# Performance work log

Measured on AMD Instinct MI355X. Metric: run time of the kernel, lower is better.

Reference implementation:

```python
import jax, jax.numpy as jnp
import numpy as np

EPS = 1e-6


def _normalize(A):
    # zero the diagonal, then symmetric degree normalization D @ A @ D.
    # D is diagonal with 1/(eps + sqrt(rowsum)), so D@A@D is an
    # elementwise row/column scale (same math, no NxN diag matmuls).
    N = A.shape[-1]
    A = A * (1.0 - jnp.eye(N, dtype=A.dtype))          # [B,N,N]
    d = 1.0 / (EPS + jnp.sqrt(jnp.sum(A, axis=2)))     # [B,N]
    return d[:, :, None] * A * d[:, None, :]           # [B,N,N]


def setup_inputs() -> dict:
    key = jax.random.key(0)
    k1, k2, k3, k4 = jax.random.split(key, 4)
    B, N, F, K, out_dim = 16, 2048, 64, 4, 128
    X = jax.random.uniform(k1, (B, N, F), dtype=jnp.float32)
    A = jax.random.uniform(k2, (B, N, N), dtype=jnp.float32)
    kernel = jax.random.normal(k3, (K * F, out_dim), dtype=jnp.float32) * 0.05
    bias = jax.random.normal(k4, (out_dim,), dtype=jnp.float32) * 0.05
    return {"X": X, "A": A, "kernel": kernel, "bias": bias}


def reference(X, A, kernel, bias):
    K = 4
    L = _normalize(A)                                  # [B,N,N]
    Xt = [X, jnp.matmul(L, X)]                         # T0, T1
    for k in range(2, K):
        Xt.append(2.0 * jnp.matmul(L, Xt[k - 1]) - Xt[k - 2])
    out = jnp.concatenate(Xt, axis=-1)                 # [B,N,K*F]
    out = jnp.matmul(out, kernel) + bias               # [B,N,out_dim]
    return jax.nn.relu(out)
```

## Files before the change

### kernel.cpp

```cpp
#include <hip/hip_runtime.h>

typedef __attribute__((ext_vector_type(4))) float  f32x4;
typedef __attribute__((ext_vector_type(8))) short  bf16x8;
typedef __attribute__((ext_vector_type(4))) int    i32x4;
typedef __attribute__((ext_vector_type(4))) unsigned short u16x4;
typedef __attribute__((ext_vector_type(8))) unsigned short u16x8;

#define NB 16
#define NN 2048
#define FF 64

#define INV_SCALE (1.0f / (127.0f * 131072.0f))

__device__ __forceinline__ unsigned short f2bf(float x) {
  union { float f; unsigned int u; } c; c.f = x;
  unsigned int u = c.u;
  return (unsigned short)((u + 0x7fffu + ((u >> 16) & 1u)) >> 16);
}
__device__ __forceinline__ float bf2f(unsigned short b) {
  union { unsigned int u; float f; } c; c.u = (unsigned int)b << 16;
  return c.f;
}

__device__ __forceinline__ void gload16(const void* g, void* l) {
  __builtin_amdgcn_global_load_lds(
      (const __attribute__((address_space(1))) void*)g,
      (__attribute__((address_space(3))) void*)l, 16, 0, 0);
}

#define BAR() asm volatile("s_barrier" ::: "memory")

__global__ __launch_bounds__(256) void rowsum_conv_kernel(
    const float* __restrict__ A, char* __restrict__ A8,
    float* __restrict__ dvec) {
  int row = blockIdx.x * 4 + (threadIdx.x >> 6);
  int lane = threadIdx.x & 63;
  int i = row & (NN - 1);
  const float* arow = A + (size_t)row * NN;
  char* orow = A8 + (size_t)row * NN;
  float s = 0.f;
#pragma unroll
  for (int p = 0; p < 8; ++p) {
    int base = p * 256 + lane * 4;
    f32x4 v = __builtin_nontemporal_load((const f32x4*)(arow + base));
#pragma unroll
    for (int jj = 0; jj < 4; ++jj) if (base + jj == i) v[jj] = 0.f;
    s += v[0] + v[1] + v[2] + v[3];
    unsigned int q0 = (unsigned int)(int)rintf(v[0] * 127.f);
    unsigned int q1 = (unsigned int)(int)rintf(v[1] * 127.f);
    unsigned int q2 = (unsigned int)(int)rintf(v[2] * 127.f);
    unsigned int q3 = (unsigned int)(int)rintf(v[3] * 127.f);
    unsigned int w8 = (q0 & 255u) | ((q1 & 255u) << 8) |
                      ((q2 & 255u) << 16) | ((q3 & 255u) << 24);
    *(unsigned int*)(orow + base) = w8;
  }
#pragma unroll
  for (int off = 32; off > 0; off >>= 1) s += __shfl_down(s, off, 64);
  if (lane == 0) dvec[row] = 1.0f / (1e-6f + sqrtf(s));
}

__global__ __launch_bounds__(256) void scale_transpose_kernel(
    const float* __restrict__ V, const float* __restrict__ dvec,
    char* __restrict__ Uh, char* __restrict__ Ul,
    unsigned short* __restrict__ Tb,
    const float* __restrict__ Kr, unsigned short* __restrict__ WT) {
  int bid = blockIdx.x;
  int tid = threadIdx.x;
  if (bid >= 512) {
    int idx = (bid - 512) * 256 + tid;
    int k = idx >> 7, c = idx & 127;
    WT[c * 256 + k] = f2bf(Kr[idx]);
    return;
  }
  int b = bid >> 5;
  int n0 = (bid & 31) * 64;
  __shared__ float t[64][65];
#pragma unroll
  for (int it = 0; it < 4; ++it) {
    int e = it * 256 + tid;
    int nl = e >> 4;
    int f0 = (e & 15) * 4;
    int n = n0 + nl;
    f32x4 v = *(const f32x4*)&V[((size_t)b * NN + n) * FF + f0];
    float dd = dvec[b * NN + n];
    u16x4 o;
#pragma unroll
    for (int j = 0; j < 4; ++j) { o[j] = f2bf(v[j]); t[f0 + j][nl] = v[j] * dd; }
    *(u16x4*)&Tb[((size_t)b * NN + n) * FF + f0] = o;
  }
  __syncthreads();
#pragma unroll
  for (int it = 0; it < 2; ++it) {
    int c = it * 256 + tid;
    int f = c >> 3, nl0 = (c & 7) * 8;
    unsigned long long ph = 0, pl = 0;
#pragma unroll
    for (int j = 0; j < 8; ++j) {
      int q = (int)rintf(t[f][nl0 + j] * 131072.f);
      q = q > 16383 ? 16383 : (q < -16383 ? -16383 : q);
      ph |= (unsigned long long)((unsigned int)(q >> 7) & 255u) << (8 * j);
      pl |= (unsigned long long)((unsigned int)(q & 127)) << (8 * j);
    }
    size_t o = ((size_t)b * FF + f) * NN + n0 + nl0;
    *(unsigned long long*)&Uh[o] = ph;
    *(unsigned long long*)&Ul[o] = pl;
  }
}

__global__ __launch_bounds__(256) void cheb_mm_kernel(
    const char* __restrict__ A8,
    const char* __restrict__ Uh,
    const char* __restrict__ Ul,
    const float* __restrict__ dvec,
    const unsigned short* __restrict__ prevb,
    unsigned short* __restrict__ Tbout,
    char* __restrict__ Uhout,
    char* __restrict__ Ulout,
    float cs) {
  __shared__ char lds[36864];
  int bid = blockIdx.x;
  int slot = bid >> 3;
  int b = (bid & 7) * 2 + (slot >> 5);
  int tm = slot & 31;
  int tid = threadIdx.x;
  int lane = tid & 63;
  int w = tid >> 6;
  int wm = w >> 1, wn = w & 1;
  int lr = lane >> 2;
  int gs = (lane & 3) ^ (lr & 3);
  int r16 = lane & 15, kq = lane >> 4;
  const int NT = NN / 64;

  const size_t abase = ((size_t)b * NN + (size_t)tm * 64) * NN;
  const size_t ubase = (size_t)b * FF * NN;

  i32x4 ach[2][2] = {};
  i32x4 acl[2][2] = {};

  auto stage = [&](int s, int kt) {
    int k0 = kt * 64;
    int r = w * 16 + lr;
    gload16(A8 + abase + (size_t)r * NN + k0 + gs * 16,
            &lds[s * 4096 + w * 1024]);
    gload16(Uh + ubase + (size_t)r * NN + k0 + gs * 16,
            &lds[12288 + s * 4096 + w * 1024]);
    gload16(Ul + ubase + (size_t)r * NN + k0 + gs * 16,
            &lds[24576 + s * 4096 + w * 1024]);
  };

  stage(0, 0); stage(1, 1); stage(2, 2);
  int s = 0;
  for (int t = 0; t < NT; ++t) {
    if (t < NT - 2)       asm volatile("s_waitcnt vmcnt(6)" ::: "memory");
    else if (t == NT - 2) asm volatile("s_waitcnt vmcnt(3)" ::: "memory");
    else                  asm volatile("s_waitcnt vmcnt(0)" ::: "memory");
    BAR();
    i32x4 af[2], uhf[2], ulf[2];
#pragma unroll
    for (int mi = 0; mi < 2; ++mi) {
      int row = wm * 32 + mi * 16 + r16;
      af[mi] = *(const i32x4*)&lds[s * 4096 + row * 64 + ((kq ^ (row & 3)) * 16)];
    }
#pragma unroll
    for (int ni = 0; ni < 2; ++ni) {
      int fr = wn * 32 + ni * 16 + r16;
      uhf[ni] = *(const i32x4*)&lds[12288 + s * 4096 + fr * 64 + ((kq ^ (fr & 3)) * 16)];
      ulf[ni] = *(const i32x4*)&lds[24576 + s * 4096 + fr * 64 + ((kq ^ (fr & 3)) * 16)];
    }
#pragma unroll
    for (int mi = 0; mi < 2; ++mi)
#pragma unroll
      for (int ni = 0; ni < 2; ++ni) {
        ach[mi][ni] = __builtin_amdgcn_mfma_i32_16x16x64_i8(
            af[mi], uhf[ni], ach[mi][ni], 0, 0, 0);
        acl[mi][ni] = __builtin_amdgcn_mfma_i32_16x16x64_i8(
            af[mi], ulf[ni], acl[mi][ni], 0, 0, 0);
      }
    BAR();
    if (t + 3 < NT) stage(s, t + 3);
    s = (s == 2) ? 0 : s + 1;
  }

  char (*th)[72]  = (char(*)[72])lds;
  char (*tlo)[72] = (char(*)[72])&lds[12288];
  int n0 = tm * 64;
#pragma unroll
  for (int mi = 0; mi < 2; ++mi) {
#pragma unroll
    for (int r = 0; r < 4; ++r) {
      int rl = wm * 32 + mi * 16 + kq * 4 + r;
      int row = n0 + rl;
      float dd = dvec[b * NN + row];
      float dcs = dd * cs;
#pragma unroll
      for (int ni = 0; ni < 2; ++ni) {
        int col = wn * 32 + ni * 16 + r16;
        size_t idx = ((size_t)b * NN + row) * FF + col;
        float c = 128.f * (float)ach[mi][ni][r] + (float)acl[mi][ni][r];
        float v = dcs * c;
        if (prevb) v -= bf2f(prevb[idx]);
        Tbout[idx] = f2bf(v);
        if (Uhout) {
          int q = (int)rintf(dd * v * 131072.f);
          q = q > 16383 ? 16383 : (q < -16383 ? -16383 : q);
          th[col][rl]  = (char)(q >> 7);
          tlo[col][rl] = (char)(q & 127);
        }
      }
    }
  }
  if (Uhout) {
    __syncthreads();
#pragma unroll
    for (int it = 0; it < 2; ++it) {
      int c = tid + it * 256;
      int f = c >> 3, nl0 = (c & 7) * 8;
      unsigned long long vh = *(const unsigned long long*)&th[f][nl0];
      unsigned long long vl = *(const unsigned long long*)&tlo[f][nl0];
      size_t o = ((size_t)b * FF + f) * NN + n0 + nl0;
      *(unsigned long long*)&Uhout[o] = vh;
      *(unsigned long long*)&Ulout[o] = vl;
    }
  }
}

__global__ __launch_bounds__(256) void final_gemm_kernel(
    const unsigned short* __restrict__ Tb,
    const unsigned short* __restrict__ WT,
    const float* __restrict__ bias,
    float* __restrict__ out) {
  __shared__ unsigned short lds[36864];
  const int M = NB * NN;
  int m0 = blockIdx.x * 64;
  int tid = threadIdx.x;
  int lane = tid & 63, w = tid >> 6;
  int wm = w >> 1, wn = w & 1;
  int lr = lane >> 3, gs = (lane & 7) ^ lr;
  int r16 = lane & 15, kq = lane >> 4;

  f32x4 acc[2][4] = {};

  auto stage = [&](int s, int kt) {
    const unsigned short* asrc = Tb + (size_t)kt * M * FF;
#pragma unroll
    for (int i = 0; i < 2; ++i) {
      int chunk = w * 2 + i;
      int r = chunk * 8 + lr;
      gload16(asrc + (size_t)(m0 + r) * FF + gs * 8,
              &lds[s * 4096 + chunk * 512]);
    }
#pragma unroll
    for (int i = 0; i < 4; ++i) {
      int chunk = w * 4 + i;
      int c = chunk * 8 + lr;
      gload16(WT + c * 256 + kt * 64 + gs * 8,
              &lds[12288 + s * 8192 + chunk * 512]);
    }
  };

  stage(0, 0); stage(1, 1); stage(2, 2);
  int s = 0;
  for (int t = 0; t < 4; ++t) {
    if (t < 2)       asm volatile("s_waitcnt vmcnt(12)" ::: "memory");
    else if (t == 2) asm volatile("s_waitcnt vmcnt(6)" ::: "memory");
    else             asm volatile("s_waitcnt vmcnt(0)" ::: "memory");
    BAR();
    bf16x8 af[2][2], bfr[4][2];
#pragma unroll
    for (int ks = 0; ks < 2; ++ks) {
#pragma unroll
      for (int mi = 0; mi < 2; ++mi) {
        int row = wm * 32 + mi * 16 + r16;
        af[mi][ks] = *(const bf16x8*)&lds[s * 4096 + row * 64 +
                                          (((ks * 4 + kq) ^ (row & 7)) * 8)];
      }
#pragma unroll
      for (int ni = 0; ni < 4; ++ni) {
        int fr = wn * 64 + ni * 16 + r16;
        bfr[ni][ks] = *(const bf16x8*)&lds[12288 + s * 8192 + fr * 64 +
                                           (((ks * 4 + kq) ^ (fr & 7)) * 8)];
      }
    }
#pragma unroll
    for (int ks = 0; ks < 2; ++ks)
#pragma unroll
      for (int mi = 0; mi < 2; ++mi)
#pragma unroll
        for (int ni = 0; ni < 4; ++ni)
          acc[mi][ni] = __builtin_amdgcn_mfma_f32_16x16x32_bf16(
              af[mi][ks], bfr[ni][ks], acc[mi][ni], 0, 0, 0);
    BAR();
    if (t + 3 < 4) stage(s, t + 3);
    s = (s == 2) ? 0 : s + 1;
  }

#pragma unroll
  for (int mi = 0; mi < 2; ++mi) {
#pragma unroll
    for (int r = 0; r < 4; ++r) {
      int row = m0 + wm * 32 + mi * 16 + kq * 4 + r;
#pragma unroll
      for (int ni = 0; ni < 4; ++ni) {
        int col = wn * 64 + ni * 16 + r16;
        float v = acc[mi][ni][r] + bias[col];
        out[(size_t)row * 128 + col] = v > 0.f ? v : 0.f;
      }
    }
  }
}

extern "C" void kernel_launch(void* const* d_in, const int* in_sizes, int n_in,
                              void* d_out, int out_size, void* d_ws, size_t ws_size,
                              hipStream_t stream) {
  const float* X    = (const float*)d_in[0];
  const float* A    = (const float*)d_in[1];
  const float* Kr   = (const float*)d_in[2];
  const float* bias = (const float*)d_in[3];
  float* out = (float*)d_out;
  char* ws = (char*)d_ws;

  const size_t SZ_A8 = (size_t)NB * NN * NN;
  const size_t SZ_D  = (size_t)NB * NN * 4;
  const size_t SZ_U  = (size_t)NB * FF * NN;
  const size_t SZ_TB = (size_t)NB * NN * FF * 2;
  const size_t TBE   = (size_t)NB * NN * FF;

  char*           A8  = ws;
  float*          dv  = (float*)(ws + SZ_A8);
  char*           Uha = ws + SZ_A8 + SZ_D;
  char*           Ula = Uha + SZ_U;
  char*           Uhb = Ula + SZ_U;
  char*           Ulb = Uhb + SZ_U;
  unsigned short* Tb  = (unsigned short*)(Ulb + SZ_U);
  unsigned short* WT  = (unsigned short*)(Ulb + SZ_U + 4 * SZ_TB);

  rowsum_conv_kernel<<<NB * NN / 4, 256, 0, stream>>>(A, A8, dv);
  scale_transpose_kernel<<<640, 256, 0, stream>>>(X, dv, Uha, Ula, Tb, Kr, WT);
  cheb_mm_kernel<<<512, 256, 0, stream>>>(A8, Uha, Ula, dv, nullptr,
                                          Tb + TBE, Uhb, Ulb, 1.0f * INV_SCALE);
  cheb_mm_kernel<<<512, 256, 0, stream>>>(A8, Uhb, Ulb, dv, Tb,
                                          Tb + 2 * TBE, Uha, Ula, 2.0f * INV_SCALE);
  cheb_mm_kernel<<<512, 256, 0, stream>>>(A8, Uha, Ula, dv, Tb + TBE,
                                          Tb + 3 * TBE, nullptr, nullptr, 2.0f * INV_SCALE);
  final_gemm_kernel<<<512, 256, 0, stream>>>(Tb, WT, bias, out);
}
```

Before: 137.2 us.

## Deepen cheb matmul pipeline to four stages and streamline int8 quantization

The Chebyshev int8 MFMA matmul kernel now keeps four LDS stages in flight instead of three. LDS grows to 48KB and the vmcnt waits are rebuilt to match, so more global-load latency can be hidden. The rowsum/quantize kernel now loads 8 floats per lane and quantizes with a magic-number FMA plus byte permutes instead of rintf and shifts. The diagonal is handled after the loop by subtracting it from the row sum and zeroing that byte, rather than a per-element compare. The larger LDS footprint may lower occupancy, and the magic-constant rounding assumes non-negative inputs in [0,1].

```diff
diff --git a/kernel.cpp b/kernel.cpp
--- a/kernel.cpp
+++ b/kernel.cpp
@@ -4,7 +4,7 @@
 typedef __attribute__((ext_vector_type(8))) short  bf16x8;
 typedef __attribute__((ext_vector_type(4))) int    i32x4;
 typedef __attribute__((ext_vector_type(4))) unsigned short u16x4;
-typedef __attribute__((ext_vector_type(8))) unsigned short u16x8;
+typedef __attribute__((ext_vector_type(2))) unsigned int   u32x2;
 
 #define NB 16
 #define NN 2048
@@ -20,6 +20,9 @@
 __device__ __forceinline__ float bf2f(unsigned short b) {
   union { unsigned int u; float f; } c; c.u = (unsigned int)b << 16;
   return c.f;
+}
+__device__ __forceinline__ unsigned int fbits(float x) {
+  union { float f; unsigned int u; } c; c.f = x; return c.u;
 }
 
 __device__ __forceinline__ void gload16(const void* g, void* l) {
@@ -38,25 +41,34 @@
   int i = row & (NN - 1);
   const float* arow = A + (size_t)row * NN;
   char* orow = A8 + (size_t)row * NN;
+  float diagval = __builtin_nontemporal_load(arow + i);
   float s = 0.f;
 #pragma unroll
-  for (int p = 0; p < 8; ++p) {
-    int base = p * 256 + lane * 4;
-    f32x4 v = __builtin_nontemporal_load((const f32x4*)(arow + base));
-#pragma unroll
-    for (int jj = 0; jj < 4; ++jj) if (base + jj == i) v[jj] = 0.f;
-    s += v[0] + v[1] + v[2] + v[3];
-    unsigned int q0 = (unsigned int)(int)rintf(v[0] * 127.f);
-    unsigned int q1 = (unsigned int)(int)rintf(v[1] * 127.f);
-    unsigned int q2 = (unsigned int)(int)rintf(v[2] * 127.f);
-    unsigned int q3 = (unsigned int)(int)rintf(v[3] * 127.f);
-    unsigned int w8 = (q0 & 255u) | ((q1 & 255u) << 8) |
-                      ((q2 & 255u) << 16) | ((q3 & 255u) << 24);
-    *(unsigned int*)(orow + base) = w8;
+  for (int p = 0; p < 4; ++p) {
+    int base = p * 512 + lane * 8;
+    f32x4 v0 = __builtin_nontemporal_load((const f32x4*)(arow + base));
+    f32x4 v1 = __builtin_nontemporal_load((const f32x4*)(arow + base + 4));
+    s += v0[0] + v0[1] + v0[2] + v0[3] + v1[0] + v1[1] + v1[2] + v1[3];
+    float y0 = fmaf(v0[0], 127.f, 8388608.f), y1 = fmaf(v0[1], 127.f, 8388608.f);
+    float y2 = fmaf(v0[2], 127.f, 8388608.f), y3 = fmaf(v0[3], 127.f, 8388608.f);
+    float y4 = fmaf(v1[0], 127.f, 8388608.f), y5 = fmaf(v1[1], 127.f, 8388608.f);
+    float y6 = fmaf(v1[2], 127.f, 8388608.f), y7 = fmaf(v1[3], 127.f, 8388608.f);
+    unsigned p01 = __builtin_amdgcn_perm(fbits(y1), fbits(y0), 0x0C0C0400u);
+    unsigned p23 = __builtin_amdgcn_perm(fbits(y3), fbits(y2), 0x0C0C0400u);
+    unsigned p45 = __builtin_amdgcn_perm(fbits(y5), fbits(y4), 0x0C0C0400u);
+    unsigned p67 = __builtin_amdgcn_perm(fbits(y7), fbits(y6), 0x0C0C0400u);
+    u32x2 w;
+    w[0] = __builtin_amdgcn_perm(p23, p01, 0x05040100u);
+    w[1] = __builtin_amdgcn_perm(p67, p45, 0x05040100u);
+    *(u32x2*)(orow + base) = w;
   }
 #pragma unroll
   for (int off = 32; off > 0; off >>= 1) s += __shfl_down(s, off, 64);
-  if (lane == 0) dvec[row] = 1.0f / (1e-6f + sqrtf(s));
+  asm volatile("s_waitcnt vmcnt(0)" ::: "memory");
+  if (lane == 0) {
+    orow[i] = 0;
+    dvec[row] = 1.0f / (1e-6f + sqrtf(s - diagval));
+  }
 }
 
 __global__ __launch_bounds__(256) void scale_transpose_kernel(
@@ -117,7 +129,7 @@
     char* __restrict__ Uhout,
     char* __restrict__ Ulout,
     float cs) {
-  __shared__ char lds[36864];
+  __shared__ char lds[49152];
   int bid = blockIdx.x;
   int slot = bid >> 3;
   int b = (bid & 7) * 2 + (slot >> 5);
@@ -143,15 +155,16 @@
     gload16(A8 + abase + (size_t)r * NN + k0 + gs * 16,
             &lds[s * 4096 + w * 1024]);
     gload16(Uh + ubase + (size_t)r * NN + k0 + gs * 16,
-            &lds[12288 + s * 4096 + w * 1024]);
+            &lds[16384 + s * 4096 + w * 1024]);
     gload16(Ul + ubase + (size_t)r * NN + k0 + gs * 16,
-            &lds[24576 + s * 4096 + w * 1024]);
+            &lds[32768 + s * 4096 + w * 1024]);
   };
 
-  stage(0, 0); stage(1, 1); stage(2, 2);
+  stage(0, 0); stage(1, 1); stage(2, 2); stage(3, 3);
   int s = 0;
   for (int t = 0; t < NT; ++t) {
-    if (t < NT - 2)       asm volatile("s_waitcnt vmcnt(6)" ::: "memory");
+    if (t < NT - 3)       asm volatile("s_waitcnt vmcnt(9)" ::: "memory");
+    else if (t == NT - 3) asm volatile("s_waitcnt vmcnt(6)" ::: "memory");
     else if (t == NT - 2) asm volatile("s_waitcnt vmcnt(3)" ::: "memory");
     else                  asm volatile("s_waitcnt vmcnt(0)" ::: "memory");
     BAR();
@@ -164,8 +177,8 @@
 #pragma unroll
     for (int ni = 0; ni < 2; ++ni) {
       int fr = wn * 32 + ni * 16 + r16;
-      uhf[ni] = *(const i32x4*)&lds[12288 + s * 4096 + fr * 64 + ((kq ^ (fr & 3)) * 16)];
-      ulf[ni] = *(const i32x4*)&lds[24576 + s * 4096 + fr * 64 + ((kq ^ (fr & 3)) * 16)];
+      uhf[ni] = *(const i32x4*)&lds[16384 + s * 4096 + fr * 64 + ((kq ^ (fr & 3)) * 16)];
+      ulf[ni] = *(const i32x4*)&lds[32768 + s * 4096 + fr * 64 + ((kq ^ (fr & 3)) * 16)];
     }
 #pragma unroll
     for (int mi = 0; mi < 2; ++mi)
@@ -177,12 +190,12 @@
             af[mi], ulf[ni], acl[mi][ni], 0, 0, 0);
       }
     BAR();
-    if (t + 3 < NT) stage(s, t + 3);
-    s = (s == 2) ? 0 : s + 1;
+    if (t + 4 < NT) stage(s, t + 4);
+    s = (s + 1) & 3;
   }
 
   char (*th)[72]  = (char(*)[72])lds;
-  char (*tlo)[72] = (char(*)[72])&lds[12288];
+  char (*tlo)[72] = (char(*)[72])&lds[16384];
   int n0 = tm * 64;
 #pragma unroll
   for (int mi = 0; mi < 2; ++mi) {
```

Result: slower. 144.8 us (+5.5%).
